# Performance work log

Measured on AMD Instinct MI355X. Metric: run time of the kernel, lower is better.

Reference implementation:

```python
import jax, jax.numpy as jnp
import numpy as np

B, C, H, W = 8, 64, 256, 512
FOV = np.pi / 4.0
KH = KW = 3


def _sphere_indices(H, W, fov):
    """Nearest-neighbor gather indices for a 3x3 spherical (gnomonic) kernel
    of angular extent `fov` on an equirectangular grid. Returns int32 [H, W, 9]."""
    taps = [(p, q) for p in (-1, 0, 1) for q in (-1, 0, 1)]
    theta = (0.5 - (np.arange(H) + 0.5) / H) * np.pi            # latitude per row [H]
    phi = ((np.arange(W) + 0.5) / W - 0.5) * 2.0 * np.pi        # longitude per col [W]
    r = np.tan(fov / 2.0)                                       # tangent-plane half extent
    gi_l, gj_l = [], []
    for (p, q) in taps:
        y_t, x_t = p * r, q * r
        rho = np.hypot(x_t, y_t)
        if rho == 0.0:
            lat = theta
            lon_off = np.zeros_like(theta)
        else:
            nu = np.arctan(rho)
            lat = np.arcsin(np.clip(np.cos(nu) * np.sin(theta)
                                    + y_t * np.sin(nu) * np.cos(theta) / rho, -1.0, 1.0))
            lon_off = np.arctan2(x_t * np.sin(nu),
                                 rho * np.cos(theta) * np.cos(nu)
                                 - y_t * np.sin(theta) * np.sin(nu))
        lon = phi[None, :] + lon_off[:, None]                   # [H, W]
        gi = np.clip(np.round((0.5 - lat / np.pi) * H - 0.5), 0, H - 1).astype(np.int32)
        gi = np.broadcast_to(gi[:, None], (H, W)).copy()
        gj = (np.round((lon / (2.0 * np.pi) + 0.5) * W - 0.5).astype(np.int64) % W).astype(np.int32)
        gi_l.append(gi)
        gj_l.append(gj)
    return np.stack(gi_l, axis=-1), np.stack(gj_l, axis=-1)    # [H, W, 9] each


def setup_inputs() -> dict:
    key = jax.random.key(0)
    k1, k2 = jax.random.split(key)
    feature = jax.random.normal(k1, (B, C, H, W), dtype=jnp.float32)
    weight = jax.random.normal(k2, (1, C, KH, KW), dtype=jnp.float32) * 0.05
    gi, gj = _sphere_indices(H, W, FOV)
    return {"feature": feature, "weight": weight,
            "gi": jnp.asarray(gi), "gj": jnp.asarray(gj)}


def reference(feature, weight, gi, gj):
    # SphericalConv: gather-based 3x3 conv over spherical sampling grid, stride 1, no bias.
    O, Cc, kh, kw = weight.shape
    wflat = weight.reshape(O, Cc, kh * kw)                      # [O, C, 9]
    Bb = feature.shape[0]
    Hh, Ww = gi.shape[0], gi.shape[1]
    out = jnp.zeros((Bb, O, Hh, Ww), feature.dtype)
    for k in range(kh * kw):                                    # fixed 9-tap loop
        xk = feature[:, :, gi[:, :, k], gj[:, :, k]]            # gather -> [B, C, H, W]
        out = out + jnp.einsum('bchw,oc->bohw', xk, wflat[:, :, k])
    # nn.Upsample(scale_factor=2) default nearest
    return jnp.repeat(jnp.repeat(out, 2, axis=2), 2, axis=3)
```

## Files before the change

kernel.cpp:

```cpp
#include <hip/hip_runtime.h>

#define Bn   8
#define Cn   64
#define Hn   256
#define Wn   512
#define HWn  (Hn * Wn)
#define TAPS 9
#define BH   4

typedef float vfloat2 __attribute__((ext_vector_type(2)));

__global__ __launch_bounds__(256, 4) void pass1_chandot(
    const float* __restrict__ feat, const float* __restrict__ wt,
    float* __restrict__ D)
{
    const int strip = blockIdx.x & 511;
    const int half  = blockIdx.x >> 9;
    const int p     = strip * 256 + (int)threadIdx.x;
    const float* fbase = feat + (size_t)half * BH * Cn * HWn + p;

    float acc[TAPS][BH];
#pragma unroll
    for (int k = 0; k < TAPS; ++k)
#pragma unroll
        for (int b = 0; b < BH; ++b) acc[k][b] = 0.f;

    float buf[2][4][BH];

#pragma unroll
    for (int ci = 0; ci < 4; ++ci)
#pragma unroll
        for (int b = 0; b < BH; ++b)
            buf[0][ci][b] = __builtin_nontemporal_load(
                fbase + (size_t)(b * Cn + ci) * HWn);

#pragma unroll
    for (int g = 0; g < 16; ++g) {
        const int cur = g & 1, nxt = cur ^ 1;
        if (g < 15) {
            const int c0 = (g + 1) * 4;
#pragma unroll
            for (int ci = 0; ci < 4; ++ci)
#pragma unroll
                for (int b = 0; b < BH; ++b)
                    buf[nxt][ci][b] = __builtin_nontemporal_load(
                        fbase + (size_t)(b * Cn + c0 + ci) * HWn);
        }
#pragma unroll
        for (int ci = 0; ci < 4; ++ci) {
            const int c = g * 4 + ci;
#pragma unroll
            for (int k = 0; k < TAPS; ++k) {
                const float wv = wt[c * TAPS + k];
#pragma unroll
                for (int b = 0; b < BH; ++b)
                    acc[k][b] = fmaf(buf[cur][ci][b], wv, acc[k][b]);
            }
        }
    }

#pragma unroll
    for (int k = 0; k < TAPS; ++k) {
        float4* dst = (float4*)(D + ((size_t)(k * 2 + half) * HWn + p) * BH);
        *dst = make_float4(acc[k][0], acc[k][1], acc[k][2], acc[k][3]);
    }
}

__global__ __launch_bounds__(256) void pass2_gather(
    const float* __restrict__ D, const int* __restrict__ gi,
    const int* __restrict__ gj, float* __restrict__ out)
{
    __shared__ int loff[256 * TAPS];
    const int tid   = threadIdx.x;
    const int p0    = blockIdx.x * 256;
    const int gbase = p0 * TAPS;

#pragma unroll
    for (int i = tid; i < 256 * TAPS; i += 256)
        loff[i] = gi[gbase + i] * Wn + gj[gbase + i];
    __syncthreads();

    const int p = p0 + tid;
    const int w = p & (Wn - 1);
    const int h = p >> 9;

    int off[TAPS];
#pragma unroll
    for (int k = 0; k < TAPS; ++k) off[k] = loff[tid * TAPS + k];

    float4 x0[TAPS], x1[TAPS];
#pragma unroll
    for (int k = 0; k < TAPS; ++k) {
        x0[k] = *(const float4*)(D + ((size_t)(2 * k)     * HWn + off[k]) * BH);
        x1[k] = *(const float4*)(D + ((size_t)(2 * k + 1) * HWn + off[k]) * BH);
    }

    float a[Bn];
#pragma unroll
    for (int b = 0; b < Bn; ++b) a[b] = 0.f;
#pragma unroll
    for (int k = 0; k < TAPS; ++k) {
        a[0] += x0[k].x; a[1] += x0[k].y; a[2] += x0[k].z; a[3] += x0[k].w;
        a[4] += x1[k].x; a[5] += x1[k].y; a[6] += x1[k].z; a[7] += x1[k].w;
    }

#pragma unroll
    for (int b = 0; b < Bn; ++b) {
        vfloat2 vv = {a[b], a[b]};
        size_t o = ((size_t)b * (2 * Hn) + 2 * h) * (size_t)(2 * Wn) + 2 * w;
        __builtin_nontemporal_store(vv, (vfloat2*)(out + o));
        __builtin_nontemporal_store(vv, (vfloat2*)(out + o + 2 * Wn));
    }
}

__global__ __launch_bounds__(256) void direct_kernel(
    const float* __restrict__ feat, const float* __restrict__ wt,
    const int* __restrict__ gi, const int* __restrict__ gj,
    float* __restrict__ out)
{
    int p = blockIdx.x * blockDim.x + threadIdx.x;
    int w = p & (Wn - 1);
    int h = (p >> 9) & (Hn - 1);
    int b = p >> 17;

    int iidx = ((h << 9) | w) * TAPS;
    int off[TAPS];
#pragma unroll
    for (int k = 0; k < TAPS; ++k)
        off[k] = gi[iidx + k] * Wn + gj[iidx + k];

    float acc = 0.f;
    for (int c = 0; c < Cn; ++c) {
        const float* fc = feat + ((size_t)b * Cn + c) * HWn;
#pragma unroll
        for (int k = 0; k < TAPS; ++k)
            acc = fmaf(fc[off[k]], wt[c * TAPS + k], acc);
    }

    float2 v = make_float2(acc, acc);
    size_t o0 = ((size_t)b * (2 * Hn) + 2 * h) * (size_t)(2 * Wn) + 2 * w;
    *(float2*)(out + o0)          = v;
    *(float2*)(out + o0 + 2 * Wn) = v;
}

extern "C" void kernel_launch(void* const* d_in, const int* in_sizes, int n_in,
                              void* d_out, int out_size, void* d_ws, size_t ws_size,
                              hipStream_t stream) {
    const float* feat = (const float*)d_in[0];
    const float* wt   = (const float*)d_in[1];
    const int*   gi   = (const int*)d_in[2];
    const int*   gj   = (const int*)d_in[3];
    float*       out  = (float*)d_out;

    const size_t bytesD = (size_t)TAPS * 2 * HWn * BH * sizeof(float);

    if (ws_size >= bytesD) {
        float* D = (float*)d_ws;
        pass1_chandot<<<2 * (HWn / 256), 256, 0, stream>>>(feat, wt, D);
        pass2_gather <<<HWn / 256, 256, 0, stream>>>(D, gi, gj, out);
    } else {
        direct_kernel<<<(Bn * HWn) / 256, 256, 0, stream>>>(feat, wt, gi, gj, out);
    }
}
```

Measured before the change: 364.6 us.

## Fuse channel-dot and gather passes into one cooperative kernel with grid sync

Combines the two passes into a single cooperatively launched kernel. Each block computes both batch halves of the channel-weighted tap sums, then all blocks meet at a grid-wide barrier before doing the gathered 9-tap sum and the 2x nearest upsample store. The aim is to remove the second kernel launch and the gap between the passes. The cost is fewer resident blocks: a grid of 512 blocks at two blocks per CU gives less memory-level parallelism than the previous 1024-block first pass. If the cooperative launch is rejected, the code falls back to the old two-kernel path.

```diff
diff --git a/kernel.cpp b/kernel.cpp
--- a/kernel.cpp
+++ b/kernel.cpp
@@ -1,4 +1,7 @@
 #include <hip/hip_runtime.h>
+#include <hip/hip_cooperative_groups.h>
+
+namespace cg = cooperative_groups;
 
 #define Bn   8
 #define Cn   64
@@ -10,6 +13,108 @@
 
 typedef float vfloat2 __attribute__((ext_vector_type(2)));
 
+__global__ __launch_bounds__(256, 2) void fused_kernel(
+    const float* __restrict__ feat, const float* __restrict__ wt,
+    const int* __restrict__ gi, const int* __restrict__ gj,
+    float* __restrict__ D, float* __restrict__ out)
+{
+    const int tid = threadIdx.x;
+    const int blk = blockIdx.x;
+    const int p   = blk * 256 + tid;
+
+    for (int half = 0; half < 2; ++half) {
+        const float* fbase = feat + (size_t)half * BH * Cn * HWn + p;
+
+        float acc[TAPS][BH];
+#pragma unroll
+        for (int k = 0; k < TAPS; ++k)
+#pragma unroll
+            for (int b = 0; b < BH; ++b) acc[k][b] = 0.f;
+
+        float buf[2][4][BH];
+
+#pragma unroll
+        for (int ci = 0; ci < 4; ++ci)
+#pragma unroll
+            for (int b = 0; b < BH; ++b)
+                buf[0][ci][b] = __builtin_nontemporal_load(
+                    fbase + (size_t)(b * Cn + ci) * HWn);
+
+#pragma unroll
+        for (int g = 0; g < 16; ++g) {
+            const int cur = g & 1, nxt = cur ^ 1;
+            if (g < 15) {
+                const int c0 = (g + 1) * 4;
+#pragma unroll
+                for (int ci = 0; ci < 4; ++ci)
+#pragma unroll
+                    for (int b = 0; b < BH; ++b)
+                        buf[nxt][ci][b] = __builtin_nontemporal_load(
+                            fbase + (size_t)(b * Cn + c0 + ci) * HWn);
+            }
+#pragma unroll
+            for (int ci = 0; ci < 4; ++ci) {
+                const int c = g * 4 + ci;
+#pragma unroll
+                for (int k = 0; k < TAPS; ++k) {
+                    const float wv = wt[c * TAPS + k];
+#pragma unroll
+                    for (int b = 0; b < BH; ++b)
+                        acc[k][b] = fmaf(buf[cur][ci][b], wv, acc[k][b]);
+                }
+            }
+        }
+
+#pragma unroll
+        for (int k = 0; k < TAPS; ++k) {
+            float4* dst = (float4*)(D + ((size_t)(k * 2 + half) * HWn + p) * BH);
+            *dst = make_float4(acc[k][0], acc[k][1], acc[k][2], acc[k][3]);
+        }
+    }
+
+    cg::this_grid().sync();
+
+    __shared__ int loff[256 * TAPS];
+    const int p0    = blk * 256;
+    const int gbase = p0 * TAPS;
+
+#pragma unroll
+    for (int i = tid; i < 256 * TAPS; i += 256)
+        loff[i] = gi[gbase + i] * Wn + gj[gbase + i];
+    __syncthreads();
+
+    const int w = p & (Wn - 1);
+    const int h = p >> 9;
+
+    int off[TAPS];
+#pragma unroll
+    for (int k = 0; k < TAPS; ++k) off[k] = loff[tid * TAPS + k];
+
+    float4 x0[TAPS], x1[TAPS];
+#pragma unroll
+    for (int k = 0; k < TAPS; ++k) {
+        x0[k] = *(const float4*)(D + ((size_t)(2 * k)     * HWn + off[k]) * BH);
+        x1[k] = *(const float4*)(D + ((size_t)(2 * k + 1) * HWn + off[k]) * BH);
+    }
+
+    float a[Bn];
+#pragma unroll
+    for (int b = 0; b < Bn; ++b) a[b] = 0.f;
+#pragma unroll
+    for (int k = 0; k < TAPS; ++k) {
+        a[0] += x0[k].x; a[1] += x0[k].y; a[2] += x0[k].z; a[3] += x0[k].w;
+        a[4] += x1[k].x; a[5] += x1[k].y; a[6] += x1[k].z; a[7] += x1[k].w;
+    }
+
+#pragma unroll
+    for (int b = 0; b < Bn; ++b) {
+        vfloat2 vv = {a[b], a[b]};
+        size_t o = ((size_t)b * (2 * Hn) + 2 * h) * (size_t)(2 * Wn) + 2 * w;
+        __builtin_nontemporal_store(vv, (vfloat2*)(out + o));
+        __builtin_nontemporal_store(vv, (vfloat2*)(out + o + 2 * Wn));
+    }
+}
+
 __global__ __launch_bounds__(256, 4) void pass1_chandot(
     const float* __restrict__ feat, const float* __restrict__ wt,
     float* __restrict__ D)
@@ -26,7 +131,6 @@
         for (int b = 0; b < BH; ++b) acc[k][b] = 0.f;
 
     float buf[2][4][BH];
-
 #pragma unroll
     for (int ci = 0; ci < 4; ++ci)
 #pragma unroll
@@ -156,8 +260,14 @@
 
     if (ws_size >= bytesD) {
         float* D = (float*)d_ws;
-        pass1_chandot<<<2 * (HWn / 256), 256, 0, stream>>>(feat, wt, D);
-        pass2_gather <<<HWn / 256, 256, 0, stream>>>(D, gi, gj, out);
+        void* args[] = {(void*)&feat, (void*)&wt, (void*)&gi, (void*)&gj,
+                        (void*)&D, (void*)&out};
+        hipError_t e = hipLaunchCooperativeKernel(
+            (const void*)fused_kernel, dim3(HWn / 256), dim3(256), args, 0, stream);
+        if (e != hipSuccess) {
+            pass1_chandot<<<2 * (HWn / 256), 256, 0, stream>>>(feat, wt, D);
+            pass2_gather <<<HWn / 256, 256, 0, stream>>>(D, gi, gj, out);
+        }
     } else {
         direct_kernel<<<(Bn * HWn) / 256, 256, 0, stream>>>(feat, wt, gi, gj, out);
     }
```

Result: slower. 479.6 us (+31.6%).
